# Performance work log

Hardware: AMD Instinct MI355X
Metric: run time of the kernel (lower is better)

Reference implementation:

```python
import jax, jax.numpy as jnp
import numpy as np

N, E = 50000, 800000
F_IN, F_OUT, H, F_EDGE = 256, 32, 8, 5
LEAKY_SLOPE = 0.2


def setup_inputs() -> dict:
    key = jax.random.key(0)
    ks = jax.random.split(key, 6)
    x = jax.random.normal(ks[0], (N, F_IN), dtype=jnp.float32)
    edge_index = jax.random.randint(ks[1], (2, E), 0, N, dtype=jnp.int64)
    edge_attr = jax.random.normal(ks[2], (E, F_EDGE), dtype=jnp.float32)
    degree_src = jax.random.randint(ks[3], (E,), 0, 64, dtype=jnp.int64)
    # Xavier-uniform params
    lim_W = float(np.sqrt(6.0 / (F_IN + F_OUT)))
    W = jax.random.uniform(ks[4], (H, F_IN, F_OUT), minval=-lim_W, maxval=lim_W, dtype=jnp.float32)
    A = 2 * F_OUT + F_EDGE
    lim_a = float(np.sqrt(6.0 / (H + A)))
    a = jax.random.uniform(ks[5], (H, A), minval=-lim_a, maxval=lim_a, dtype=jnp.float32)
    lim_e = float(np.sqrt(1.0 / F_EDGE))
    W_edge_w = jax.random.uniform(jax.random.fold_in(key, 7), (F_EDGE, F_EDGE), minval=-lim_e, maxval=lim_e, dtype=jnp.float32)
    return {"x": x, "edge_index": edge_index, "edge_attr": edge_attr,
            "degree_src": degree_src, "W": W, "a": a, "W_edge_w": W_edge_w}


def reference(x, edge_index, edge_attr, degree_src, W, a, W_edge_w):
    n = x.shape[0]
    h, f_out = W.shape[0], W.shape[2]
    src, dst = edge_index[0], edge_index[1]
    # per-head projection: (N, H, F_out)
    Wh = jnp.einsum('nf,hfo->nho', x, W)
    # split attention vector instead of materializing the concat
    a_src, a_dst, a_e = a[:, :f_out], a[:, f_out:2 * f_out], a[:, 2 * f_out:]
    ef = edge_attr @ W_edge_w.T                      # (E, F_edge)
    e = (jnp.einsum('eho,ho->eh', Wh[src], a_src)
         + jnp.einsum('eho,ho->eh', Wh[dst], a_dst)
         + ef @ a_e.T)                                # (E, H)
    e = jax.nn.leaky_relu(e, LEAKY_SLOPE)
    scale = 1.0 / jnp.sqrt(jnp.clip(degree_src.astype(jnp.float32), 1.0, None))
    e = e * scale[:, None]
    # segment softmax over src; torch scatter_reduce amax include_self=True with zeros init -> max includes 0
    e_max = jnp.maximum(jax.ops.segment_max(e, src, num_segments=n), 0.0)
    e_exp = jnp.exp(e - e_max[src])
    e_sum = jax.ops.segment_sum(e_exp, src, num_segments=n)
    alpha = e_exp / (e_sum[src] + 1e-16)             # (E, H)
    msg = Wh[dst] * alpha[:, :, None]                # (E, H, F_out)
    out = jax.ops.segment_sum(msg, src, num_segments=n)
    out = jax.nn.elu(out.reshape(n, h * f_out))
    return out, alpha
```

## Files before the change

kernel.cpp:

```cpp
#include <hip/hip_runtime.h>
#include <hip/hip_bf16.h>
#include <math.h>

#define NN 50000
#define NE 800000
#define FIN 256
#define FOUT 32
#define NH 8
#define FE 5
#define AROW 69
#define NROWS_PAD 50048
#define BSTRIDE 64

typedef float f32x4 __attribute__((ext_vector_type(4)));
typedef short bf16x8 __attribute__((ext_vector_type(8)));

static __device__ __forceinline__ unsigned short f2bf(float f) {
    unsigned u = __float_as_uint(f);
    unsigned r = (u + 0x7FFFu + ((u >> 16) & 1u)) >> 16;
    return (unsigned short)r;
}
static __device__ __forceinline__ float bf2f(unsigned short b) {
    return __uint_as_float(((unsigned)b) << 16);
}

__global__ __launch_bounds__(256) void k_prepre(const float* __restrict__ W,
                                                const float* __restrict__ a,
                                                const float* __restrict__ Wew,
                                                const float* __restrict__ x,
                                                const int* __restrict__ ei,
                                                float* __restrict__ C,
                                                unsigned short* __restrict__ Bh,
                                                unsigned short* __restrict__ Bsh,
                                                unsigned short* __restrict__ Bsl,
                                                unsigned short* __restrict__ xb,
                                                int* __restrict__ counts,
                                                int* __restrict__ pos) {
    int b = blockIdx.x, t = threadIdx.x;
    int i = b * 256 + t;
    if (i < (NN * FIN) / 8) {
        f32x4 u0 = *(const f32x4*)&x[(size_t)i * 8];
        f32x4 u1 = *(const f32x4*)&x[(size_t)i * 8 + 4];
        bf16x8 hi;
        hi[0] = (short)f2bf(u0.x); hi[1] = (short)f2bf(u0.y);
        hi[2] = (short)f2bf(u0.z); hi[3] = (short)f2bf(u0.w);
        hi[4] = (short)f2bf(u1.x); hi[5] = (short)f2bf(u1.y);
        hi[6] = (short)f2bf(u1.z); hi[7] = (short)f2bf(u1.w);
        *(bf16x8*)&xb[(size_t)i * 8] = hi;
    }
    if (i < NE / 4) {
        int4 e4 = *(const int4*)&ei[i * 4];
        int4 pv;
        pv.x = atomicAdd(&counts[e4.x], 1);
        pv.y = atomicAdd(&counts[e4.y], 1);
        pv.z = atomicAdd(&counts[e4.z], 1);
        pv.w = atomicAdd(&counts[e4.w], 1);
        *(int4*)&pos[i * 4] = pv;
    }
    if (b < 256) {
        int c = b, k = t;
        int h = c >> 5, o = c & 31;
        Bh[c * 256 + k] = f2bf(W[(size_t)h * (FIN * FOUT) + (size_t)k * FOUT + o]);
    } else if (b == 256) {
        if (t < NH * FE) {
            int h = t / FE, k = t % FE;
            float s = 0.f;
            for (int j = 0; j < FE; ++j) s += a[h * AROW + 2 * FOUT + j] * Wew[j * FE + k];
            C[t] = s;
        }
        int k = t;
        for (int h = 0; h < NH; ++h) {
            float s1v = 0.f, s2v = 0.f;
            for (int o = 0; o < FOUT; ++o) {
                float wv = W[(size_t)h * (FIN * FOUT) + (size_t)k * FOUT + o];
                s1v += wv * a[h * AROW + o];
                s2v += wv * a[h * AROW + FOUT + o];
            }
            unsigned short h1 = f2bf(s1v);
            Bsh[h * 256 + k] = h1;
            Bsl[h * 256 + k] = f2bf(s1v - bf2f(h1));
            unsigned short h2 = f2bf(s2v);
            Bsh[(8 + h) * 256 + k] = h2;
            Bsl[(8 + h) * 256 + k] = f2bf(s2v - bf2f(h2));
        }
    }
}

__global__ __launch_bounds__(256) void k_gemm_mfma(const unsigned short* __restrict__ xb,
                                                   const unsigned short* __restrict__ Bh,
                                                   const unsigned short* __restrict__ Bsh,
                                                   const unsigned short* __restrict__ Bsl,
                                                   unsigned short* __restrict__ Whb,
                                                   float* __restrict__ s1,
                                                   float* __restrict__ s2, int nrows) {
    int t = threadIdx.x;
    int w = t >> 6, l = t & 63;
    int r = l & 15, blk = l >> 4;
    int row0 = blockIdx.x * 32;
    int c0 = w * 64;

    f32x4 acc[2][4];
    f32x4 acc_s = (f32x4)(0.f);
#pragma unroll
    for (int i = 0; i < 2; ++i)
#pragma unroll
        for (int j = 0; j < 4; ++j) acc[i][j] = (f32x4)(0.f);

    const unsigned short* ap[2];
#pragma unroll
    for (int rt = 0; rt < 2; ++rt)
        ap[rt] = xb + (size_t)(row0 + rt * 16 + r) * 256 + blk * 8;

#pragma unroll
    for (int ks = 0; ks < 8; ++ks) {
        const int k0 = ks * 32;
        bf16x8 ah[2];
#pragma unroll
        for (int rt = 0; rt < 2; ++rt)
            ah[rt] = *(const bf16x8*)(ap[rt] + k0);
        bf16x8 bh[4];
#pragma unroll
        for (int ct = 0; ct < 4; ++ct) {
            int c = c0 + ct * 16 + r;
            bh[ct] = *(const bf16x8*)&Bh[c * 256 + k0 + blk * 8];
        }
#pragma unroll
        for (int ct = 0; ct < 4; ++ct) {
#pragma unroll
            for (int rt = 0; rt < 2; ++rt)
                acc[rt][ct] = __builtin_amdgcn_mfma_f32_16x16x32_bf16(ah[rt], bh[ct], acc[rt][ct], 0, 0, 0);
        }
        if (w < 2) {
            bf16x8 bsh = *(const bf16x8*)&Bsh[r * 256 + k0 + blk * 8];
            bf16x8 bsl = *(const bf16x8*)&Bsl[r * 256 + k0 + blk * 8];
            acc_s = __builtin_amdgcn_mfma_f32_16x16x32_bf16(ah[w], bsh, acc_s, 0, 0, 0);
            acc_s = __builtin_amdgcn_mfma_f32_16x16x32_bf16(ah[w], bsl, acc_s, 0, 0, 0);
        }
    }

#pragma unroll
    for (int rt = 0; rt < 2; ++rt) {
#pragma unroll
        for (int reg = 0; reg < 4; ++reg) {
            int row = row0 + rt * 16 + blk * 4 + reg;
            if (row < nrows) {
#pragma unroll
                for (int ct = 0; ct < 4; ++ct)
                    Whb[(size_t)row * 256 + c0 + ct * 16 + r] = f2bf(acc[rt][ct][reg]);
            }
        }
    }
    if (w < 2) {
#pragma unroll
        for (int reg = 0; reg < 4; ++reg) {
            int row = row0 + w * 16 + blk * 4 + reg;
            if (row < nrows) {
                if (r < 8) s1[row * NH + r] = acc_s[reg];
                else       s2[row * NH + (r - 8)] = acc_s[reg];
            }
        }
    }
}

__global__ __launch_bounds__(256) void k_scatlog(const int* __restrict__ ei,
                                                 const float* __restrict__ eattr,
                                                 const int* __restrict__ degs,
                                                 const float* __restrict__ s1,
                                                 const float* __restrict__ s2,
                                                 const float* __restrict__ C,
                                                 const int* __restrict__ pos,
                                                 unsigned short* __restrict__ e_perm,
                                                 int2* __restrict__ de_perm) {
    __shared__ float Cl[NH * FE];
    int t = threadIdx.x;
    if (t < NH * FE) Cl[t] = C[t];
    __syncthreads();
    int e = blockIdx.x * 256 + t;
    if (e >= NE) return;
    int src = ei[e], dst = ei[NE + e];
    int dg = degs[e];
    float scale = rsqrtf((float)(dg > 1 ? dg : 1));
    float ea0 = eattr[(size_t)e * FE + 0];
    float ea1 = eattr[(size_t)e * FE + 1];
    float ea2 = eattr[(size_t)e * FE + 2];
    float ea3 = eattr[(size_t)e * FE + 3];
    float ea4 = eattr[(size_t)e * FE + 4];
    float4 s1a = *(const float4*)&s1[src * NH];
    float4 s1b = *(const float4*)&s1[src * NH + 4];
    float4 s2a = *(const float4*)&s2[dst * NH];
    float4 s2b = *(const float4*)&s2[dst * NH + 4];
    float vs1[8] = {s1a.x, s1a.y, s1a.z, s1a.w, s1b.x, s1b.y, s1b.z, s1b.w};
    float vs2[8] = {s2a.x, s2a.y, s2a.z, s2a.w, s2b.x, s2b.y, s2b.z, s2b.w};
    bf16x8 v;
#pragma unroll
    for (int h = 0; h < NH; ++h) {
        float q = vs1[h] + vs2[h] + ea0 * Cl[h * FE + 0] + ea1 * Cl[h * FE + 1] +
                  ea2 * Cl[h * FE + 2] + ea3 * Cl[h * FE + 3] + ea4 * Cl[h * FE + 4];
        q = q > 0.f ? q : 0.2f * q;
        v[h] = (short)f2bf(q * scale);
    }
    int ps = pos[e];
    if (ps < BSTRIDE) {
        int p = src * BSTRIDE + ps;
        *(bf16x8*)&e_perm[(size_t)p * 8] = v;
        de_perm[p] = make_int2(dst, e);
    }
}

__global__ __launch_bounds__(256) void k_smmsg(const int* __restrict__ counts,
                                               const unsigned short* __restrict__ e_perm,
                                               const int2* __restrict__ de_perm,
                                               const unsigned short* __restrict__ Whb,
                                               float* __restrict__ out_alpha,
                                               float* __restrict__ out) {
    __shared__ float al[4][256];
    __shared__ int dl[4][32];
    __shared__ int el[4][32];
    int t = threadIdx.x;
    int w = t >> 6, l = t & 63;
    int n = blockIdx.x * 4 + w;
    if (n >= NN) return;
    int start = n * BSTRIDE;
    int deg = counts[n];
    if (deg > BSTRIDE) deg = BSTRIDE;
    int j = l >> 3, h = l & 7;

    float vc[4];
#pragma unroll
    for (int q = 0; q < 4; ++q) {
        int b = j + 8 * q;
        vc[q] = (b < deg) ? bf2f(e_perm[(size_t)(start + b) * 8 + h]) : -1e30f;
    }
    float mx = 0.f;
#pragma unroll
    for (int q = 0; q < 4; ++q) mx = fmaxf(mx, vc[q]);
    for (int b = 32 + j; b < deg; b += 8)
        mx = fmaxf(mx, bf2f(e_perm[(size_t)(start + b) * 8 + h]));
    mx = fmaxf(mx, __shfl_xor(mx, 8));
    mx = fmaxf(mx, __shfl_xor(mx, 16));
    mx = fmaxf(mx, __shfl_xor(mx, 32));
    float m = mx;
    float ex[4];
    float sm = 0.f;
#pragma unroll
    for (int q = 0; q < 4; ++q) { ex[q] = __expf(vc[q] - m); sm += ex[q]; }
    for (int b = 32 + j; b < deg; b += 8)
        sm += __expf(bf2f(e_perm[(size_t)(start + b) * 8 + h]) - m);
    sm += __shfl_xor(sm, 8);
    sm += __shfl_xor(sm, 16);
    sm += __shfl_xor(sm, 32);
    float inv = 1.f / (sm + 1e-16f);
    f32x4 acc = (f32x4)(0.f);
    int hh = l >> 3;
    for (int base = 0; base < deg; base += 32) {
        int cnt = deg - base;
        if (cnt > 32) cnt = 32;
        if (l < cnt) {
            int2 de = de_perm[start + base + l];
            dl[w][l] = de.x;
            el[w][l] = de.y;
        }
        asm volatile("s_waitcnt lgkmcnt(0)" ::: "memory");
#pragma unroll
        for (int q = 0; q < 4; ++q) {
            int b = base + j + 8 * q;
            if (b < deg) {
                float av = (base == 0 ? ex[q]
                                      : __expf(bf2f(e_perm[(size_t)(start + b) * 8 + h]) - m)) * inv;
                al[w][(j + 8 * q) * 8 + h] = av;
                out_alpha[(size_t)el[w][j + 8 * q] * 8 + h] = av;
            }
        }
        asm volatile("s_waitcnt lgkmcnt(0)" ::: "memory");
        int jj = 0;
        for (; jj + 2 <= cnt; jj += 2) {
            int d0 = dl[w][jj], d1 = dl[w][jj + 1];
            float a0 = al[w][jj * 8 + hh], a1 = al[w][jj * 8 + 8 + hh];
            ushort4 u0 = *(const ushort4*)&Whb[(size_t)d0 * 256 + l * 4];
            ushort4 u1 = *(const ushort4*)&Whb[(size_t)d1 * 256 + l * 4];
            acc.x += a0 * bf2f(u0.x) + a1 * bf2f(u1.x);
            acc.y += a0 * bf2f(u0.y) + a1 * bf2f(u1.y);
            acc.z += a0 * bf2f(u0.z) + a1 * bf2f(u1.z);
            acc.w += a0 * bf2f(u0.w) + a1 * bf2f(u1.w);
        }
        if (jj < cnt) {
            int d0 = dl[w][jj];
            float a0 = al[w][jj * 8 + hh];
            ushort4 u0 = *(const ushort4*)&Whb[(size_t)d0 * 256 + l * 4];
            acc.x += a0 * bf2f(u0.x);
            acc.y += a0 * bf2f(u0.y);
            acc.z += a0 * bf2f(u0.z);
            acc.w += a0 * bf2f(u0.w);
        }
        asm volatile("s_waitcnt lgkmcnt(0)" ::: "memory");
    }
    f32x4 o;
    o.x = acc.x > 0.f ? acc.x : expm1f(acc.x);
    o.y = acc.y > 0.f ? acc.y : expm1f(acc.y);
    o.z = acc.z > 0.f ? acc.z : expm1f(acc.z);
    o.w = acc.w > 0.f ? acc.w : expm1f(acc.w);
    *(f32x4*)&out[(size_t)n * 256 + l * 4] = o;
}

extern "C" void kernel_launch(void* const* d_in, const int* in_sizes, int n_in,
                              void* d_out, int out_size, void* d_ws, size_t ws_size,
                              hipStream_t stream) {
    const float* x     = (const float*)d_in[0];
    const int*   ei    = (const int*)d_in[1];
    const float* eattr = (const float*)d_in[2];
    const int*   degs  = (const int*)d_in[3];
    const float* W     = (const float*)d_in[4];
    const float* a     = (const float*)d_in[5];
    const float* Wew   = (const float*)d_in[6];

    float* out       = (float*)d_out;
    float* out_alpha = out + (size_t)NN * 256;

    char* p = (char*)d_ws;
    auto alloc = [&](size_t bytes) -> char* {
        char* r = p;
        p += (bytes + 255) & ~(size_t)255;
        return r;
    };
    unsigned short* Whb     = (unsigned short*)alloc((size_t)NN * 256 * 2);
    unsigned short* xb      = (unsigned short*)alloc((size_t)NROWS_PAD * 256 * 2);
    float*          s1      = (float*)alloc((size_t)NN * NH * 4);
    float*          s2      = (float*)alloc((size_t)NN * NH * 4);
    float*          Cm      = (float*)alloc(NH * FE * 4);
    unsigned short* Bh      = (unsigned short*)alloc((size_t)256 * 256 * 2);
    unsigned short* Bsh     = (unsigned short*)alloc((size_t)16 * 256 * 2);
    unsigned short* Bsl     = (unsigned short*)alloc((size_t)16 * 256 * 2);
    int*            counts  = (int*)alloc((size_t)NN * 4);
    int*            pos     = (int*)alloc((size_t)NE * 4);
    unsigned short* e_perm  = (unsigned short*)alloc(((size_t)NN * BSTRIDE + 64) * NH * 2);
    int2*           de_perm = (int2*)alloc(((size_t)NN * BSTRIDE + 64) * 8);

    hipMemsetAsync(counts, 0, (size_t)NN * 4, stream);

    k_prepre<<<(NN * FIN / 8 + 255) / 256, 256, 0, stream>>>(W, a, Wew, x, ei, Cm, Bh,
                                                             Bsh, Bsl, xb, counts, pos);
    k_gemm_mfma<<<NROWS_PAD / 32, 256, 0, stream>>>(xb, Bh, Bsh, Bsl, Whb, s1, s2, NN);
    k_scatlog<<<(NE + 255) / 256, 256, 0, stream>>>(ei, eattr, degs, s1, s2, Cm,
                                                    pos, e_perm, de_perm);
    k_smmsg<<<(NN + 3) / 4, 256, 0, stream>>>(counts, e_perm, de_perm, Whb,
                                              out_alpha, out);
}
```

Before: 232.6 us.

## Fuse x bf16 conversion into GEMM, shrink bucket stride, unroll message loop by 4

Removes the standalone fp32-to-bf16 conversion of x from the prep kernel and converts on the fly inside the MFMA GEMM, eliminating a full write and re-read of the bf16 copy. The per-node edge bucket stride is reduced from 64 to 48 to shrink the permuted edge buffers. The message aggregation loop is unrolled to four neighbor rows per iteration for more memory-level parallelism. The GEMM now reads twice the bytes for x, and the smaller bucket stride assumes max degree stays within 48.

```diff
diff --git a/kernel.cpp b/kernel.cpp
--- a/kernel.cpp
+++ b/kernel.cpp
@@ -10,7 +10,7 @@
 #define FE 5
 #define AROW 69
 #define NROWS_PAD 50048
-#define BSTRIDE 64
+#define BSTRIDE 48
 
 typedef float f32x4 __attribute__((ext_vector_type(4)));
 typedef short bf16x8 __attribute__((ext_vector_type(8)));
@@ -23,31 +23,23 @@
 static __device__ __forceinline__ float bf2f(unsigned short b) {
     return __uint_as_float(((unsigned)b) << 16);
 }
+static __device__ __forceinline__ short f2bf_fast(float f) {
+    __hip_bfloat16 h = __float2bfloat16(f);
+    return *reinterpret_cast<short*>(&h);
+}
 
 __global__ __launch_bounds__(256) void k_prepre(const float* __restrict__ W,
                                                 const float* __restrict__ a,
                                                 const float* __restrict__ Wew,
-                                                const float* __restrict__ x,
                                                 const int* __restrict__ ei,
                                                 float* __restrict__ C,
                                                 unsigned short* __restrict__ Bh,
                                                 unsigned short* __restrict__ Bsh,
                                                 unsigned short* __restrict__ Bsl,
-                                                unsigned short* __restrict__ xb,
                                                 int* __restrict__ counts,
                                                 int* __restrict__ pos) {
     int b = blockIdx.x, t = threadIdx.x;
     int i = b * 256 + t;
-    if (i < (NN * FIN) / 8) {
-        f32x4 u0 = *(const f32x4*)&x[(size_t)i * 8];
-        f32x4 u1 = *(const f32x4*)&x[(size_t)i * 8 + 4];
-        bf16x8 hi;
-        hi[0] = (short)f2bf(u0.x); hi[1] = (short)f2bf(u0.y);
-        hi[2] = (short)f2bf(u0.z); hi[3] = (short)f2bf(u0.w);
-        hi[4] = (short)f2bf(u1.x); hi[5] = (short)f2bf(u1.y);
-        hi[6] = (short)f2bf(u1.z); hi[7] = (short)f2bf(u1.w);
-        *(bf16x8*)&xb[(size_t)i * 8] = hi;
-    }
     if (i < NE / 4) {
         int4 e4 = *(const int4*)&ei[i * 4];
         int4 pv;
@@ -86,7 +78,7 @@
     }
 }
 
-__global__ __launch_bounds__(256) void k_gemm_mfma(const unsigned short* __restrict__ xb,
+__global__ __launch_bounds__(256) void k_gemm_mfma(const float* __restrict__ x,
                                                    const unsigned short* __restrict__ Bh,
                                                    const unsigned short* __restrict__ Bsh,
                                                    const unsigned short* __restrict__ Bsl,
@@ -106,18 +98,27 @@
 #pragma unroll
         for (int j = 0; j < 4; ++j) acc[i][j] = (f32x4)(0.f);
 
-    const unsigned short* ap[2];
-#pragma unroll
-    for (int rt = 0; rt < 2; ++rt)
-        ap[rt] = xb + (size_t)(row0 + rt * 16 + r) * 256 + blk * 8;
+    const float* ap[2];
+#pragma unroll
+    for (int rt = 0; rt < 2; ++rt) {
+        int row = row0 + rt * 16 + r;
+        if (row >= nrows) row = nrows - 1;
+        ap[rt] = x + (size_t)row * 256 + blk * 8;
+    }
 
 #pragma unroll
     for (int ks = 0; ks < 8; ++ks) {
         const int k0 = ks * 32;
         bf16x8 ah[2];
 #pragma unroll
-        for (int rt = 0; rt < 2; ++rt)
-            ah[rt] = *(const bf16x8*)(ap[rt] + k0);
+        for (int rt = 0; rt < 2; ++rt) {
+            f32x4 u0 = *(const f32x4*)(ap[rt] + k0);
+            f32x4 u1 = *(const f32x4*)(ap[rt] + k0 + 4);
+            ah[rt][0] = f2bf_fast(u0.x); ah[rt][1] = f2bf_fast(u0.y);
+            ah[rt][2] = f2bf_fast(u0.z); ah[rt][3] = f2bf_fast(u0.w);
+            ah[rt][4] = f2bf_fast(u1.x); ah[rt][5] = f2bf_fast(u1.y);
+            ah[rt][6] = f2bf_fast(u1.z); ah[rt][7] = f2bf_fast(u1.w);
+        }
         bf16x8 bh[4];
 #pragma unroll
         for (int ct = 0; ct < 4; ++ct) {
@@ -273,17 +274,20 @@
         }
         asm volatile("s_waitcnt lgkmcnt(0)" ::: "memory");
         int jj = 0;
-        for (; jj + 2 <= cnt; jj += 2) {
-            int d0 = dl[w][jj], d1 = dl[w][jj + 1];
-            float a0 = al[w][jj * 8 + hh], a1 = al[w][jj * 8 + 8 + hh];
+        for (; jj + 4 <= cnt; jj += 4) {
+            int d0 = dl[w][jj], d1 = dl[w][jj + 1], d2 = dl[w][jj + 2], d3 = dl[w][jj + 3];
+            float a0 = al[w][jj * 8 + hh],      a1 = al[w][jj * 8 + 8 + hh];
+            float a2 = al[w][jj * 8 + 16 + hh], a3 = al[w][jj * 8 + 24 + hh];
             ushort4 u0 = *(const ushort4*)&Whb[(size_t)d0 * 256 + l * 4];
             ushort4 u1 = *(const ushort4*)&Whb[(size_t)d1 * 256 + l * 4];
-            acc.x += a0 * bf2f(u0.x) + a1 * bf2f(u1.x);
-            acc.y += a0 * bf2f(u0.y) + a1 * bf2f(u1.y);
-            acc.z += a0 * bf2f(u0.z) + a1 * bf2f(u1.z);
-            acc.w += a0 * bf2f(u0.w) + a1 * bf2f(u1.w);
-        }
-        if (jj < cnt) {
+            ushort4 u2 = *(const ushort4*)&Whb[(size_t)d2 * 256 + l * 4];
+            ushort4 u3 = *(const ushort4*)&Whb[(size_t)d3 * 256 + l * 4];
+            acc.x += a0 * bf2f(u0.x) + a1 * bf2f(u1.x) + a2 * bf2f(u2.x) + a3 * bf2f(u3.x);
+            acc.y += a0 * bf2f(u0.y) + a1 * bf2f(u1.y) + a2 * bf2f(u2.y) + a3 * bf2f(u3.y);
+            acc.z += a0 * bf2f(u0.z) + a1 * bf2f(u1.z) + a2 * bf2f(u2.z) + a3 * bf2f(u3.z);
+            acc.w += a0 * bf2f(u0.w) + a1 * bf2f(u1.w) + a2 * bf2f(u2.w) + a3 * bf2f(u3.w);
+        }
+        for (; jj < cnt; ++jj) {
             int d0 = dl[w][jj];
             float a0 = al[w][jj * 8 + hh];
             ushort4 u0 = *(const ushort4*)&Whb[(size_t)d0 * 256 + l * 4];
@@ -323,7 +327,6 @@
         return r;
     };
     unsigned short* Whb     = (unsigned short*)alloc((size_t)NN * 256 * 2);
-    unsigned short* xb      = (unsigned short*)alloc((size_t)NROWS_PAD * 256 * 2);
     float*          s1      = (float*)alloc((size_t)NN * NH * 4);
     float*          s2      = (float*)alloc((size_t)NN * NH * 4);
     float*          Cm      = (float*)alloc(NH * FE * 4);
@@ -337,9 +340,9 @@
 
     hipMemsetAsync(counts, 0, (size_t)NN * 4, stream);
 
-    k_prepre<<<(NN * FIN / 8 + 255) / 256, 256, 0, stream>>>(W, a, Wew, x, ei, Cm, Bh,
-                                                             Bsh, Bsl, xb, counts, pos);
-    k_gemm_mfma<<<NROWS_PAD / 32, 256, 0, stream>>>(xb, Bh, Bsh, Bsl, Whb, s1, s2, NN);
+    k_prepre<<<(NE / 4 + 255) / 256, 256, 0, stream>>>(W, a, Wew, ei, Cm, Bh,
+                                                       Bsh, Bsl, counts, pos);
+    k_gemm_mfma<<<NROWS_PAD / 32, 256, 0, stream>>>(x, Bh, Bsh, Bsl, Whb, s1, s2, NN);
     k_scatlog<<<(NE + 255) / 256, 256, 0, stream>>>(ei, eattr, degs, s1, s2, Cm,
                                                     pos, e_perm, de_perm);
     k_smmsg<<<(NN + 3) / 4, 256, 0, stream>>>(counts, e_perm, de_perm, Whb,
```

After: 223.1 us. 1.04x faster.
